# Performance work log

Hardware: AMD Instinct MI355X
Metric: run time of the kernel (lower is better)

The kernel has to match this reference:

```python
import jax, jax.numpy as jnp
import numpy as np

N = 65536  # number of 3D query points
H = 60     # hidden width


def setup_inputs() -> dict:
    key = jax.random.key(0)
    ks = jax.random.split(key, 11)
    return {
        "x": jax.random.normal(ks[0], (N, 3), jnp.float32),
        "w1": jax.random.normal(ks[1], (H, 3), jnp.float32) * 0.5,
        "b1": jax.random.normal(ks[2], (H,), jnp.float32) * 0.1,
        "w2": jax.random.normal(ks[3], (H, H), jnp.float32) * 0.13,
        "b2": jax.random.normal(ks[4], (H,), jnp.float32) * 0.1,
        "w3": jax.random.normal(ks[5], (H, H), jnp.float32) * 0.13,
        "b3": jax.random.normal(ks[6], (H,), jnp.float32) * 0.1,
        "w4": jax.random.normal(ks[7], (H, H), jnp.float32) * 0.13,
        "b4": jax.random.normal(ks[8], (H,), jnp.float32) * 0.1,
        "w5": jax.random.normal(ks[9], (1, H), jnp.float32) * 0.13,
        "b5": jax.random.normal(ks[10], (1,), jnp.float32) * 0.1,
    }


def reference(x, w1, b1, w2, b2, w3, b3, w4, b4, w5, b5):
    # Batched version of the per-point ChairMLP forward.
    # neuron_state(x, W, b) builds diag(s) @ [W|b] with s = (relu_out != 0);
    # diag(s) @ W == W * s[:, None], so the whole thing is a row mask.
    # wl_k = W_k.T * s_k (cols masked), bias_k = b_k * s_k.
    # Chained products P_k = wl1 @ ... @ wl_k and B_k = affine bias chain are
    # computed without materializing [N,60,60] per-sample matrices:
    #   P_k = (P_{k-1} @ W_k.T) * s_k = alk_k_w * s_k
    #   B_k = (B_{k-1} @ W_k.T + b_k) * s_k = alk_k_b * s_k
    n = x.shape[0]
    dt = x.dtype

    h1 = jax.nn.relu(x @ w1.T + b1)                      # [N,60]
    s1 = (h1 > 0).astype(dt)
    P1 = w1.T[None, :, :] * s1[:, None, :]               # [N,3,60]
    B1 = b1 * s1                                          # [N,60]
    alk1 = jnp.broadcast_to(
        jnp.concatenate([w1.T, b1[None, :]], axis=0), (n, 4, H))

    h2 = jax.nn.relu(h1 @ w2.T + b2)
    s2 = (h2 > 0).astype(dt)
    alk2_w = jnp.einsum('nij,kj->nik', P1, w2)           # [N,3,60]
    alk2_b = B1 @ w2.T + b2                              # [N,60]
    alk2 = jnp.concatenate([alk2_w, alk2_b[:, None, :]], axis=1)
    P2 = alk2_w * s2[:, None, :]
    B2 = alk2_b * s2

    h3 = jax.nn.relu(h2 @ w3.T + b3)
    s3 = (h3 > 0).astype(dt)
    alk3_w = jnp.einsum('nij,kj->nik', P2, w3)
    alk3_b = B2 @ w3.T + b3
    alk3 = jnp.concatenate([alk3_w, alk3_b[:, None, :]], axis=1)
    P3 = alk3_w * s3[:, None, :]
    B3 = alk3_b * s3

    h4 = jax.nn.relu(h3 @ w4.T + b4)
    s4 = (h4 > 0).astype(dt)
    alk4_w = jnp.einsum('nij,kj->nik', P3, w4)
    alk4_b = B3 @ w4.T + b4
    alk4 = jnp.concatenate([alk4_w, alk4_b[:, None, :]], axis=1)
    P4 = alk4_w * s4[:, None, :]
    B4 = alk4_b * s4

    out = h4 @ w5.T + b5                                  # [N,1]
    zs_w = jnp.einsum('nij,kj->nik', P4, w5)             # [N,3,1]
    zs_b = B4 @ w5.T + b5                                 # [N,1]
    zerosurface = jnp.concatenate([zs_w, zs_b[:, None, :]], axis=1)  # [N,4,1]

    S = jnp.stack([s1, s2, s3, s4], axis=1)               # [N,4,60] == S.t() per sample
    return out, S, alk1, alk2, alk3, alk4, zerosurface
```

## Files before the change

kernel.cpp:

```cpp
#include <hip/hip_runtime.h>


constexpr int  NP = 65536;
constexpr int  HD = 60;
constexpr long CH = (long)NP * 4 * HD;
constexpr long OFF_OUT  = 0;
constexpr long OFF_S    = NP;
constexpr long OFF_ALK1 = OFF_S    + CH;
constexpr long OFF_ZS   = OFF_ALK1 + 4 * CH;

__global__ __launch_bounds__(256) void chair_fused(
    const float* __restrict__ x,
    const float* __restrict__ w1, const float* __restrict__ b1,
    const float* __restrict__ w2, const float* __restrict__ b2,
    const float* __restrict__ w3, const float* __restrict__ b3,
    const float* __restrict__ w4, const float* __restrict__ b4,
    const float* __restrict__ w5, const float* __restrict__ b5,
    float* __restrict__ out)
{
    __shared__ float hb[2][64][68];

    const int tid = threadIdx.x;
    const int lp  = tid >> 2;
    const int r   = tid & 3;
    const int n   = blockIdx.x * 64 + lp;
    const long t  = (long)n * 4 + r;
    const bool isb = (r == 3);
    float* Sp = out + OFF_S + (long)n * (4 * HD);

    const float x0 = x[3*n+0], x1 = x[3*n+1], x2 = x[3*n+2];
#pragma unroll
    for (int jj = 0; jj < 15; ++jj) {
        const int j = 4*jj + r;
        float acc = b1[j];
        acc = fmaf(x0, w1[3*j+0], acc);
        acc = fmaf(x1, w1[3*j+1], acc);
        acc = fmaf(x2, w1[3*j+2], acc);
        Sp[j] = acc > 0.f ? 1.f : 0.f;
        hb[1][lp][j] = acc > 0.f ? acc : 0.f;
    }
    __syncthreads();

    float row[60];
    {
        float* alkp = out + OFF_ALK1 + t * HD;
#pragma unroll
        for (int c0 = 0; c0 < 60; c0 += 4) {
            float4 wv;
            wv.x = isb ? b1[c0+0] : w1[3*(c0+0) + r];
            wv.y = isb ? b1[c0+1] : w1[3*(c0+1) + r];
            wv.z = isb ? b1[c0+2] : w1[3*(c0+2) + r];
            wv.w = isb ? b1[c0+3] : w1[3*(c0+3) + r];
            *reinterpret_cast<float4*>(alkp + c0) = wv;
            float4 hp = *reinterpret_cast<const float4*>(&hb[1][lp][c0]);
            row[c0+0] = hp.x > 0.f ? wv.x : 0.f;
            row[c0+1] = hp.y > 0.f ? wv.y : 0.f;
            row[c0+2] = hp.z > 0.f ? wv.z : 0.f;
            row[c0+3] = hp.w > 0.f ? wv.w : 0.f;
        }
    }

    float zacc = isb ? b5[0] : 0.f;

#pragma unroll 1
    for (int k = 2; k <= 4; ++k) {
        const float* __restrict__ W = (k == 2) ? w2 : ((k == 3) ? w3 : w4);
        const float* __restrict__ B = (k == 2) ? b2 : ((k == 3) ? b3 : b4);
        const int bc = k & 1;
        const int bp = (k - 1) & 1;
        float*       alkc = out + OFF_ALK1 + (long)(k-1) * CH + t * HD;
        const float* alkp = out + OFF_ALK1 + (long)(k-2) * CH + t * HD;

        __syncthreads();

        {
            float h[60];
#pragma unroll
            for (int c0 = 0; c0 < 60; c0 += 4)
                *reinterpret_cast<float4*>(&h[c0]) =
                    *reinterpret_cast<const float4*>(&hb[bp][lp][c0]);
            float* Sk = Sp + (k-1) * HD;
#pragma unroll 1
            for (int jj = 0; jj < 15; ++jj) {
                const int j = 4*jj + r;
                float acc = B[j];
                const float* wr = W + j * HD;
#pragma unroll
                for (int c0 = 0; c0 < 60; c0 += 4) {
                    float4 wv = *reinterpret_cast<const float4*>(wr + c0);
                    acc = fmaf(h[c0+0], wv.x, acc);
                    acc = fmaf(h[c0+1], wv.y, acc);
                    acc = fmaf(h[c0+2], wv.z, acc);
                    acc = fmaf(h[c0+3], wv.w, acc);
                }
                Sk[j] = acc > 0.f ? 1.f : 0.f;
                hb[bc][lp][j] = acc > 0.f ? acc : 0.f;
            }
        }
        __syncthreads();

#pragma unroll
        for (int c0 = 0; c0 < 60; c0 += 4) {
            float4 a  = *reinterpret_cast<const float4*>(alkp + c0);
            float4 hp = *reinterpret_cast<const float4*>(&hb[bp][lp][c0]);
            row[c0+0] = hp.x > 0.f ? a.x : 0.f;
            row[c0+1] = hp.y > 0.f ? a.y : 0.f;
            row[c0+2] = hp.z > 0.f ? a.z : 0.f;
            row[c0+3] = hp.w > 0.f ? a.w : 0.f;
        }

#pragma unroll 1
        for (int j0 = 0; j0 < 60; j0 += 12) {
            float acc[12];
#pragma unroll
            for (int jj = 0; jj < 12; ++jj) acc[jj] = isb ? B[j0+jj] : 0.f;
#pragma unroll
            for (int jj = 0; jj < 12; ++jj) {
                const float* wr = W + (j0+jj) * HD;
#pragma unroll
                for (int c = 0; c < 60; ++c)
                    acc[jj] = fmaf(row[c], wr[c], acc[jj]);
            }
#pragma unroll
            for (int jj = 0; jj < 12; jj += 4) {
                float4 v = { acc[jj], acc[jj+1], acc[jj+2], acc[jj+3] };
                *reinterpret_cast<float4*>(alkc + j0 + jj) = v;
            }
            if (k == 4) {
#pragma unroll
                for (int jj = 0; jj < 12; ++jj) {
                    float hv = hb[0][lp][j0+jj];
                    zacc = fmaf(hv > 0.f ? acc[jj] : 0.f, w5[j0+jj], zacc);
                }
            }
        }
    }

    out[OFF_ZS + t] = zacc;

    if (r == 0) {
        float acc = b5[0];
#pragma unroll
        for (int c0 = 0; c0 < 60; c0 += 4) {
            float4 hv = *reinterpret_cast<const float4*>(&hb[0][lp][c0]);
            float4 wv = *reinterpret_cast<const float4*>(w5 + c0);
            acc = fmaf(hv.x, wv.x, acc);
            acc = fmaf(hv.y, wv.y, acc);
            acc = fmaf(hv.z, wv.z, acc);
            acc = fmaf(hv.w, wv.w, acc);
        }
        out[OFF_OUT + n] = acc;
    }
}

extern "C" void kernel_launch(void* const* d_in, const int* in_sizes, int n_in,
                              void* d_out, int out_size, void* d_ws, size_t ws_size,
                              hipStream_t stream) {
    const float* x  = (const float*)d_in[0];
    const float* w1 = (const float*)d_in[1];
    const float* b1 = (const float*)d_in[2];
    const float* w2 = (const float*)d_in[3];
    const float* b2 = (const float*)d_in[4];
    const float* w3 = (const float*)d_in[5];
    const float* b3 = (const float*)d_in[6];
    const float* w4 = (const float*)d_in[7];
    const float* b4 = (const float*)d_in[8];
    const float* w5 = (const float*)d_in[9];
    const float* b5 = (const float*)d_in[10];
    float* out = (float*)d_out;

    chair_fused<<<NP / 64, 256, 0, stream>>>(
        x, w1, b1, w2, b2, w3, b3, w4, b4, w5, b5, out);
}
```

Baseline: 631.7 us.

## Keep masked alk rows in registers instead of reloading from global output

Result: slower. 726.2 us (+15.0%).

```diff
diff --git a/kernel.cpp b/kernel.cpp
--- a/kernel.cpp
+++ b/kernel.cpp
@@ -6,10 +6,10 @@
 constexpr long CH = (long)NP * 4 * HD;
 constexpr long OFF_OUT  = 0;
 constexpr long OFF_S    = NP;
-constexpr long OFF_ALK1 = OFF_S    + CH;
+constexpr long OFF_ALK1 = OFF_S + CH;
 constexpr long OFF_ZS   = OFF_ALK1 + 4 * CH;
 
-__global__ __launch_bounds__(256) void chair_fused(
+__global__ __launch_bounds__(256, 3) void chair_fused(
     const float* __restrict__ x,
     const float* __restrict__ w1, const float* __restrict__ b1,
     const float* __restrict__ w2, const float* __restrict__ b2,
@@ -68,10 +68,6 @@
         const float* __restrict__ B = (k == 2) ? b2 : ((k == 3) ? b3 : b4);
         const int bc = k & 1;
         const int bp = (k - 1) & 1;
-        float*       alkc = out + OFF_ALK1 + (long)(k-1) * CH + t * HD;
-        const float* alkp = out + OFF_ALK1 + (long)(k-2) * CH + t * HD;
-
-        __syncthreads();
 
         {
             float h[60];
@@ -83,56 +79,74 @@
 #pragma unroll 1
             for (int jj = 0; jj < 15; ++jj) {
                 const int j = 4*jj + r;
-                float acc = B[j];
                 const float* wr = W + j * HD;
+                float a0 = B[j], a1 = 0.f, a2 = 0.f, a3 = 0.f;
 #pragma unroll
-                for (int c0 = 0; c0 < 60; c0 += 4) {
-                    float4 wv = *reinterpret_cast<const float4*>(wr + c0);
-                    acc = fmaf(h[c0+0], wv.x, acc);
-                    acc = fmaf(h[c0+1], wv.y, acc);
-                    acc = fmaf(h[c0+2], wv.z, acc);
-                    acc = fmaf(h[c0+3], wv.w, acc);
+                for (int q = 0; q < 15; q += 4) {
+                    {
+                        float4 wv = *reinterpret_cast<const float4*>(wr + 4*q);
+                        a0 = fmaf(h[4*q+0], wv.x, a0); a0 = fmaf(h[4*q+1], wv.y, a0);
+                        a0 = fmaf(h[4*q+2], wv.z, a0); a0 = fmaf(h[4*q+3], wv.w, a0);
+                    }
+                    if (q + 1 < 15) {
+                        float4 wv = *reinterpret_cast<const float4*>(wr + 4*(q+1));
+                        a1 = fmaf(h[4*q+4], wv.x, a1); a1 = fmaf(h[4*q+5], wv.y, a1);
+                        a1 = fmaf(h[4*q+6], wv.z, a1); a1 = fmaf(h[4*q+7], wv.w, a1);
+                    }
+                    if (q + 2 < 15) {
+                        float4 wv = *reinterpret_cast<const float4*>(wr + 4*(q+2));
+                        a2 = fmaf(h[4*q+8],  wv.x, a2); a2 = fmaf(h[4*q+9],  wv.y, a2);
+                        a2 = fmaf(h[4*q+10], wv.z, a2); a2 = fmaf(h[4*q+11], wv.w, a2);
+                    }
+                    if (q + 3 < 15) {
+                        float4 wv = *reinterpret_cast<const float4*>(wr + 4*(q+3));
+                        a3 = fmaf(h[4*q+12], wv.x, a3); a3 = fmaf(h[4*q+13], wv.y, a3);
+                        a3 = fmaf(h[4*q+14], wv.z, a3); a3 = fmaf(h[4*q+15], wv.w, a3);
+                    }
                 }
+                float acc = (a0 + a1) + (a2 + a3);
                 Sk[j] = acc > 0.f ? 1.f : 0.f;
                 hb[bc][lp][j] = acc > 0.f ? acc : 0.f;
             }
         }
         __syncthreads();
 
+        {
+            float nrow[60];
+            float* alkc = out + OFF_ALK1 + (long)(k-1) * CH + t * HD;
+#pragma unroll 1
+            for (int j0 = 0; j0 < 60; j0 += 12) {
+                float acc[12];
 #pragma unroll
-        for (int c0 = 0; c0 < 60; c0 += 4) {
-            float4 a  = *reinterpret_cast<const float4*>(alkp + c0);
-            float4 hp = *reinterpret_cast<const float4*>(&hb[bp][lp][c0]);
-            row[c0+0] = hp.x > 0.f ? a.x : 0.f;
-            row[c0+1] = hp.y > 0.f ? a.y : 0.f;
-            row[c0+2] = hp.z > 0.f ? a.z : 0.f;
-            row[c0+3] = hp.w > 0.f ? a.w : 0.f;
-        }
-
-#pragma unroll 1
-        for (int j0 = 0; j0 < 60; j0 += 12) {
-            float acc[12];
+                for (int jj = 0; jj < 12; ++jj) acc[jj] = isb ? B[j0+jj] : 0.f;
 #pragma unroll
-            for (int jj = 0; jj < 12; ++jj) acc[jj] = isb ? B[j0+jj] : 0.f;
+                for (int jj = 0; jj < 12; ++jj) {
+                    const float* wr = W + (j0+jj) * HD;
 #pragma unroll
-            for (int jj = 0; jj < 12; ++jj) {
-                const float* wr = W + (j0+jj) * HD;
+                    for (int c = 0; c < 60; ++c)
+                        acc[jj] = fmaf(row[c], wr[c], acc[jj]);
+                }
 #pragma unroll
-                for (int c = 0; c < 60; ++c)
-                    acc[jj] = fmaf(row[c], wr[c], acc[jj]);
+                for (int jj = 0; jj < 12; jj += 4) {
+                    float4 v = { acc[jj], acc[jj+1], acc[jj+2], acc[jj+3] };
+                    *reinterpret_cast<float4*>(alkc + j0 + jj) = v;
+                }
+#pragma unroll
+                for (int jj = 0; jj < 12; ++jj) nrow[j0+jj] = acc[jj];
             }
 #pragma unroll
-            for (int jj = 0; jj < 12; jj += 4) {
-                float4 v = { acc[jj], acc[jj+1], acc[jj+2], acc[jj+3] };
-                *reinterpret_cast<float4*>(alkc + j0 + jj) = v;
+            for (int c0 = 0; c0 < 60; c0 += 4) {
+                float4 hp = *reinterpret_cast<const float4*>(&hb[bc][lp][c0]);
+                row[c0+0] = hp.x > 0.f ? nrow[c0+0] : 0.f;
+                row[c0+1] = hp.y > 0.f ? nrow[c0+1] : 0.f;
+                row[c0+2] = hp.z > 0.f ? nrow[c0+2] : 0.f;
+                row[c0+3] = hp.w > 0.f ? nrow[c0+3] : 0.f;
             }
-            if (k == 4) {
+        }
+        if (k == 4) {
 #pragma unroll
-                for (int jj = 0; jj < 12; ++jj) {
-                    float hv = hb[0][lp][j0+jj];
-                    zacc = fmaf(hv > 0.f ? acc[jj] : 0.f, w5[j0+jj], zacc);
-                }
-            }
+            for (int c = 0; c < 60; ++c)
+                zacc = fmaf(row[c], w5[c], zacc);
         }
     }
 
```
